# Performance work log

Hardware: AMD Instinct MI355X
Metric: run time of the kernel (lower is better)

Reference implementation:

```python
import jax, jax.numpy as jnp
import numpy as np

N = 262144   # occupied sparse voxels
C = 64       # channels
K3 = 27      # 3^3 kernel offsets (rulebook width)


def spconv(feats, W, nbr):
    """Submanifold sparse conv: gather -> matmul -> accumulate per kernel offset.
    feats: [N, Cin], W: [K3, Cin, Cout], nbr: [N, K3] int32 neighbor indices.
    """
    def step(acc, wi):
        w, idx = wi          # w: [Cin, Cout], idx: [N]
        return acc + feats[idx] @ w, None
    acc = jnp.zeros((feats.shape[0], W.shape[-1]), dtype=feats.dtype)
    out, _ = jax.lax.scan(step, acc, (W, nbr.T))
    return out


def inr(feats, nbr, w00, w01, w10, w11, w12):
    # branch 0: conv0_1(relu(conv0_0(x)))  (both k=3)
    out0 = spconv(jax.nn.relu(spconv(feats, w00, nbr)), w01, nbr)
    # branch 1: conv1_2(relu(conv1_1(relu(conv1_0(x)))))  (1x1, k=3, 1x1)
    out1 = jax.nn.relu(spconv(jax.nn.relu(feats @ w10), w11, nbr)) @ w12
    # concat halves back to C, residual add
    return jnp.concatenate([out0, out1], axis=1) + feats


def setup_inputs() -> dict:
    key = jax.random.key(0)
    ks = jax.random.split(key, 16)
    Ch = C // 2
    s3 = 1.0 / np.sqrt(K3 * C)
    s3h = 1.0 / np.sqrt(K3 * Ch)
    s1 = 1.0 / np.sqrt(C)
    s1h = 1.0 / np.sqrt(Ch)
    feats = jax.random.normal(ks[0], (N, C), dtype=jnp.float32)
    nbr = jax.random.randint(ks[1], (N, K3), 0, N, dtype=jnp.int32)
    w1 = jax.random.normal(ks[2], (K3, C, C), dtype=jnp.float32) * s3
    w2 = jax.random.normal(ks[3], (K3, C, C), dtype=jnp.float32) * s3
    # 3 stacked INR blocks
    b00 = jax.random.normal(ks[4], (3, K3, C, Ch), dtype=jnp.float32) * s3
    b01 = jax.random.normal(ks[5], (3, K3, Ch, Ch), dtype=jnp.float32) * s3h
    b10 = jax.random.normal(ks[6], (3, C, Ch), dtype=jnp.float32) * s1
    b11 = jax.random.normal(ks[7], (3, K3, Ch, Ch), dtype=jnp.float32) * s3h
    b12 = jax.random.normal(ks[8], (3, Ch, Ch), dtype=jnp.float32) * s1h
    return {"feats": feats, "nbr": nbr, "w1": w1, "w2": w2,
            "b00": b00, "b01": b01, "b10": b10, "b11": b11, "b12": b12}


def reference(feats, nbr, w1, w2, b00, b01, b10, b11, b12):
    x = jax.nn.relu(spconv(feats, w1, nbr))   # x = relu(conv1(x))
    h = x
    for i in range(3):
        h = inr(h, nbr, b00[i], b01[i], b10[i], b11[i], b12[i])
    out = h + x                                # block(x) + x
    return spconv(out, w2, nbr)                # conv2(out)
```

## Files before the change

### kernel.cpp

```cpp
#include <hip/hip_runtime.h>
#include <hip/hip_bf16.h>

typedef __attribute__((ext_vector_type(8))) __bf16 bf16x8;
typedef __attribute__((ext_vector_type(4))) float f32x4;

#define DEVI __device__ __forceinline__

static constexpr int NVOX = 262144;

DEVI unsigned short f2b_rne(float f) {
    unsigned int u = __float_as_uint(f);
    u = (u + 0x7fffu + ((u >> 16) & 1u)) >> 16;
    return (unsigned short)u;
}
DEVI float b2f(unsigned short h) {
    return __uint_as_float(((unsigned int)h) << 16);
}
DEVI bf16x8 ld8(const unsigned short* p) { return *reinterpret_cast<const bf16x8*>(p); }
DEVI f32x4 mfma16(bf16x8 a, bf16x8 b, f32x4 c) {
    return __builtin_amdgcn_mfma_f32_16x16x32_bf16(a, b, c, 0, 0, 0);
}

DEVI void stage16(const unsigned short* __restrict__ src, unsigned short* dst,
                  int n16, int tid, int nthr) {
    const float4* s = reinterpret_cast<const float4*>(src);
    float4* d = reinterpret_cast<float4*>(dst);
    for (int c = tid; c < n16; c += nthr) d[c] = s[c];
}


__global__ void f2b_kernel(const float* __restrict__ src, unsigned short* __restrict__ dst) {
    const size_t i = (size_t)(blockIdx.x * 256 + threadIdx.x) * 8;
    const float4 a = *reinterpret_cast<const float4*>(src + i);
    const float4 b = *reinterpret_cast<const float4*>(src + i + 4);
    union { unsigned short h[8]; uint4 v; } o;
    o.h[0] = f2b_rne(a.x); o.h[1] = f2b_rne(a.y); o.h[2] = f2b_rne(a.z); o.h[3] = f2b_rne(a.w);
    o.h[4] = f2b_rne(b.x); o.h[5] = f2b_rne(b.y); o.h[6] = f2b_rne(b.z); o.h[7] = f2b_rne(b.w);
    *reinterpret_cast<uint4*>(dst + i) = o.v;
}

__global__ void wconv_kernel(const float* __restrict__ src, unsigned short* __restrict__ dst,
                             int K, int Cin, int Cout) {
    const int KC = Cin >> 5, NT = Cout >> 4;
    const int total = K * KC * NT * 512;
    src += (size_t)blockIdx.y * K * Cin * Cout;
    dst += (size_t)blockIdx.y * total;
    for (int e = blockIdx.x * 256 + threadIdx.x; e < total; e += gridDim.x * 256) {
        const int j = e & 7;
        const int ln = (e >> 3) & 63;
        const int blob = e >> 9;
        const int nt = blob % NT;
        const int t = blob / NT;
        const int kc = t % KC;
        const int k = t / KC;
        const int cin = kc * 32 + (ln >> 4) * 8 + j;
        const int cout = nt * 16 + (ln & 15);
        dst[e] = f2b_rne(src[((size_t)k * Cin + cin) * Cout + cout]);
    }
}


template<bool RELU, bool OUTF32>
__global__ __launch_bounds__(1024)
void conv_full_kernel(const unsigned short* __restrict__ in,
                      const int* __restrict__ nbr,
                      const unsigned short* __restrict__ wf,
                      void* __restrict__ outv)
{
    __shared__ unsigned short wlds[7 * 8 * 512];
    const int tid = threadIdx.x;
    const int lane = tid & 63, wave = tid >> 6;
    const int lrow = lane & 15, lkg = lane >> 4;
    const int vb = blockIdx.x * 512 + wave * 32;

    constexpr int ID = 6;
    constexpr int GS = 3;

    const int* nrow0 = nbr + (size_t)(vb + lrow) * 27;
    const int* nrow1 = nbr + (size_t)(vb + 16 + lrow) * 27;

    int i0[ID], i1[ID];
    bf16x8 ga[GS][2][2];

#pragma unroll
    for (int t = 0; t < ID; ++t) { i0[t] = nrow0[t]; i1[t] = nrow1[t]; }
#pragma unroll
    for (int t = 0; t < 2; ++t) {
        const unsigned short* a0 = in + (size_t)i0[t] * 64 + lkg * 8;
        const unsigned short* a1 = in + (size_t)i1[t] * 64 + lkg * 8;
        ga[t][0][0] = ld8(a0); ga[t][0][1] = ld8(a0 + 32);
        ga[t][1][0] = ld8(a1); ga[t][1][1] = ld8(a1 + 32);
    }

    const f32x4 FZ = {0.f, 0.f, 0.f, 0.f};
    f32x4 acc[2][4];
#pragma unroll
    for (int m = 0; m < 2; ++m)
#pragma unroll
        for (int nt = 0; nt < 4; ++nt) acc[m][nt] = FZ;

#pragma unroll
    for (int t = 0; t < 27; ++t) {
        if (t % 7 == 0) {
            const int nk = (27 - t) < 7 ? (27 - t) : 7;
            __syncthreads();
            stage16(wf + (size_t)t * 8 * 512, wlds, nk * 8 * 64, tid, 1024);
            __syncthreads();
        }
        if (t + ID < 27) {
            i0[t % ID] = nrow0[t + ID];
            i1[t % ID] = nrow1[t + ID];
        }
        if (t + 2 < 27) {
            const int u = t + 2, s = u % GS;
            const unsigned short* a0 = in + (size_t)i0[u % ID] * 64 + lkg * 8;
            const unsigned short* a1 = in + (size_t)i1[u % ID] * 64 + lkg * 8;
            ga[s][0][0] = ld8(a0); ga[s][0][1] = ld8(a0 + 32);
            ga[s][1][0] = ld8(a1); ga[s][1][1] = ld8(a1 + 32);
        }
        const int kk = t % 7;
        const unsigned short* bl = wlds + kk * 8 * 512 + lane * 8;
        const int s = t % GS;
#pragma unroll
        for (int kc = 0; kc < 2; ++kc)
#pragma unroll
            for (int nt = 0; nt < 4; ++nt) {
                const bf16x8 bf = ld8(bl + (kc * 4 + nt) * 512);
                acc[0][nt] = mfma16(ga[s][0][kc], bf, acc[0][nt]);
                acc[1][nt] = mfma16(ga[s][1][kc], bf, acc[1][nt]);
            }
    }

#pragma unroll
    for (int m = 0; m < 2; ++m)
#pragma unroll
        for (int nt = 0; nt < 4; ++nt)
#pragma unroll
            for (int r = 0; r < 4; ++r) {
                const int v = vb + m * 16 + lkg * 4 + r;
                float val = acc[m][nt][r];
                if (RELU) val = fmaxf(val, 0.f);
                if (OUTF32)
                    reinterpret_cast<float*>(outv)[(size_t)v * 64 + nt * 16 + lrow] = val;
                else
                    reinterpret_cast<unsigned short*>(outv)[(size_t)v * 64 + nt * 16 + lrow] = f2b_rne(val);
            }
}

__global__ __launch_bounds__(1024)
void kernel_A(const unsigned short* __restrict__ h,
              const int* __restrict__ nbr,
              const unsigned short* __restrict__ b00f,
              const unsigned short* __restrict__ b10f,
              unsigned short* __restrict__ u)
{
    __shared__ unsigned short wlds[60 * 512];
    const int tid = threadIdx.x;
    const int lane = tid & 63, wave = tid >> 6;
    const int lrow = lane & 15, lkg = lane >> 4;
    const int vb = blockIdx.x * 512 + wave * 32;

    constexpr int ID = 6;
    constexpr int GS = 3;

    const int* nrow0 = nbr + (size_t)(vb + lrow) * 27;
    const int* nrow1 = nbr + (size_t)(vb + 16 + lrow) * 27;

    int i0[ID], i1[ID];
    bf16x8 ga[GS][2][2];

#pragma unroll
    for (int t = 0; t < ID; ++t) { i0[t] = nrow0[t]; i1[t] = nrow1[t]; }
#pragma unroll
    for (int t = 0; t < 2; ++t) {
        const unsigned short* a0 = h + (size_t)i0[t] * 64 + lkg * 8;
        const unsigned short* a1 = h + (size_t)i1[t] * 64 + lkg * 8;
        ga[t][0][0] = ld8(a0); ga[t][0][1] = ld8(a0 + 32);
        ga[t][1][0] = ld8(a1); ga[t][1][1] = ld8(a1 + 32);
    }

    const f32x4 FZ = {0.f, 0.f, 0.f, 0.f};
    f32x4 acc0[2][2], acc1[2][2];
#pragma unroll
    for (int m = 0; m < 2; ++m)
#pragma unroll
        for (int nt = 0; nt < 2; ++nt) { acc0[m][nt] = FZ; acc1[m][nt] = FZ; }

#pragma unroll
    for (int t = 0; t < 27; ++t) {
        if (t == 0) {
            __syncthreads();
            stage16(b00f, wlds, 14 * 4 * 64, tid, 1024);
            stage16(b10f, wlds + 56 * 512, 4 * 64, tid, 1024);
            __syncthreads();
        } else if (t == 14) {
            __syncthreads();
            stage16(b00f + (size_t)14 * 4 * 512, wlds, 13 * 4 * 64, tid, 1024);
            __syncthreads();
        }
        if (t + ID < 27) {
            i0[t % ID] = nrow0[t + ID];
            i1[t % ID] = nrow1[t + ID];
        }
        if (t + 2 < 27) {
            const int u2 = t + 2, s = u2 % GS;
            const unsigned short* a0 = h + (size_t)i0[u2 % ID] * 64 + lkg * 8;
            const unsigned short* a1 = h + (size_t)i1[u2 % ID] * 64 + lkg * 8;
            ga[s][0][0] = ld8(a0); ga[s][0][1] = ld8(a0 + 32);
            ga[s][1][0] = ld8(a1); ga[s][1][1] = ld8(a1 + 32);
        }
        const int kk = (t < 14) ? t : t - 14;
        const unsigned short* bl = wlds + kk * 4 * 512 + lane * 8;
        const int s = t % GS;
#pragma unroll
        for (int kc = 0; kc < 2; ++kc)
#pragma unroll
            for (int nt = 0; nt < 2; ++nt) {
                const bf16x8 bf = ld8(bl + (kc * 2 + nt) * 512);
                acc0[0][nt] = mfma16(ga[s][0][kc], bf, acc0[0][nt]);
                acc0[1][nt] = mfma16(ga[s][1][kc], bf, acc0[1][nt]);
            }
    }
    {
        const unsigned short* bl = wlds + 56 * 512 + lane * 8;
#pragma unroll
        for (int m = 0; m < 2; ++m) {
            const unsigned short* ar = h + (size_t)(vb + m * 16 + lrow) * 64;
#pragma unroll
            for (int kc = 0; kc < 2; ++kc) {
                const bf16x8 af = ld8(ar + kc * 32 + lkg * 8);
#pragma unroll
                for (int nt = 0; nt < 2; ++nt) {
                    const bf16x8 bf = ld8(bl + (kc * 2 + nt) * 512);
                    acc1[m][nt] = mfma16(af, bf, acc1[m][nt]);
                }
            }
        }
    }
#pragma unroll
    for (int m = 0; m < 2; ++m)
#pragma unroll
        for (int nt = 0; nt < 2; ++nt)
#pragma unroll
            for (int r = 0; r < 4; ++r) {
                const int v = vb + m * 16 + lkg * 4 + r;
                u[(size_t)v * 64 + nt * 16 + lrow] = f2b_rne(fmaxf(acc0[m][nt][r], 0.f));
                u[(size_t)v * 64 + 32 + nt * 16 + lrow] = f2b_rne(fmaxf(acc1[m][nt][r], 0.f));
            }
}

__global__ __launch_bounds__(1024)
void kernel_B(const unsigned short* __restrict__ u,
              const int* __restrict__ nbr,
              const unsigned short* __restrict__ b01f,
              const unsigned short* __restrict__ b11f,
              const unsigned short* __restrict__ b12f,
              const unsigned short* __restrict__ hres,
              const unsigned short* __restrict__ xres,
              unsigned short* __restrict__ hout)
{
    __shared__ unsigned short wlds[56 * 512];
    const int tid = threadIdx.x;
    const int lane = tid & 63, wave = tid >> 6;
    const int lrow = lane & 15, lkg = lane >> 4;
    const int vb = blockIdx.x * 512 + wave * 32;

    constexpr int ID = 6;
    constexpr int GS = 3;

    const int* nrow0 = nbr + (size_t)(vb + lrow) * 27;
    const int* nrow1 = nbr + (size_t)(vb + 16 + lrow) * 27;

    int i0[ID], i1[ID];
    bf16x8 ga[GS][2][2];

#pragma unroll
    for (int t = 0; t < ID; ++t) { i0[t] = nrow0[t]; i1[t] = nrow1[t]; }
#pragma unroll
    for (int t = 0; t < 2; ++t) {
        const unsigned short* a0 = u + (size_t)i0[t] * 64 + lkg * 8;
        const unsigned short* a1 = u + (size_t)i1[t] * 64 + lkg * 8;
        ga[t][0][0] = ld8(a0); ga[t][0][1] = ld8(a0 + 32);
        ga[t][1][0] = ld8(a1); ga[t][1][1] = ld8(a1 + 32);
    }

    const f32x4 FZ = {0.f, 0.f, 0.f, 0.f};
    f32x4 acc0[2][2], acc1[2][2];
#pragma unroll
    for (int m = 0; m < 2; ++m)
#pragma unroll
        for (int nt = 0; nt < 2; ++nt) { acc0[m][nt] = FZ; acc1[m][nt] = FZ; }

#pragma unroll
    for (int t = 0; t < 27; ++t) {
        if (t == 0) {
            __syncthreads();
            stage16(b01f, wlds, 14 * 2 * 64, tid, 1024);
            stage16(b11f, wlds + 28 * 512, 14 * 2 * 64, tid, 1024);
            __syncthreads();
        } else if (t == 14) {
            __syncthreads();
            stage16(b01f + (size_t)28 * 512, wlds, 13 * 2 * 64, tid, 1024);
            stage16(b11f + (size_t)28 * 512, wlds + 28 * 512, 13 * 2 * 64, tid, 1024);
            __syncthreads();
        }
        if (t + ID < 27) {
            i0[t % ID] = nrow0[t + ID];
            i1[t % ID] = nrow1[t + ID];
        }
        if (t + 2 < 27) {
            const int u2 = t + 2, s = u2 % GS;
            const unsigned short* a0 = u + (size_t)i0[u2 % ID] * 64 + lkg * 8;
            const unsigned short* a1 = u + (size_t)i1[u2 % ID] * 64 + lkg * 8;
            ga[s][0][0] = ld8(a0); ga[s][0][1] = ld8(a0 + 32);
            ga[s][1][0] = ld8(a1); ga[s][1][1] = ld8(a1 + 32);
        }
        const int kk = (t < 14) ? t : t - 14;
        const unsigned short* bl = wlds + lane * 8;
        const int s = t % GS;
#pragma unroll
        for (int nt = 0; nt < 2; ++nt) {
            const bf16x8 w01 = ld8(bl + (kk * 2 + nt) * 512);
            const bf16x8 w11 = ld8(bl + (28 + kk * 2 + nt) * 512);
            acc0[0][nt] = mfma16(ga[s][0][0], w01, acc0[0][nt]);
            acc0[1][nt] = mfma16(ga[s][1][0], w01, acc0[1][nt]);
            acc1[0][nt] = mfma16(ga[s][0][1], w11, acc1[0][nt]);
            acc1[1][nt] = mfma16(ga[s][1][1], w11, acc1[1][nt]);
        }
    }

    bf16x8 w12r[2];
#pragma unroll
    for (int nt = 0; nt < 2; ++nt) w12r[nt] = ld8(b12f + nt * 512 + lane * 8);

    __syncthreads();

    f32x4 out1[2][2];
    char* tb = reinterpret_cast<char*>(wlds) + wave * 1024;
#pragma unroll
    for (int m = 0; m < 2; ++m) {
#pragma unroll
        for (int nt = 0; nt < 2; ++nt)
#pragma unroll
            for (int r = 0; r < 4; ++r) {
                const int row = lkg * 4 + r;
                const int byte = (nt * 16 + lrow) * 2;
                const int off = row * 64 + (((byte >> 4) ^ (row & 3)) << 4) + (byte & 15);
                *reinterpret_cast<unsigned short*>(tb + off) = f2b_rne(fmaxf(acc1[m][nt][r], 0.f));
            }
        __syncthreads();
        const int roff = lrow * 64 + ((lkg ^ (lrow & 3)) << 4);
        const bf16x8 af2 = *reinterpret_cast<const bf16x8*>(tb + roff);
#pragma unroll
        for (int nt = 0; nt < 2; ++nt)
            out1[m][nt] = mfma16(af2, w12r[nt], FZ);
        __syncthreads();
    }

#pragma unroll
    for (int m = 0; m < 2; ++m)
#pragma unroll
        for (int nt = 0; nt < 2; ++nt)
#pragma unroll
            for (int r = 0; r < 4; ++r) {
                const int v = vb + m * 16 + lkg * 4 + r;
                const int c0 = nt * 16 + lrow;
                const int c1 = 32 + c0;
                float r0 = acc0[m][nt][r] + b2f(hres[(size_t)v * 64 + c0]);
                float r1 = out1[m][nt][r] + b2f(hres[(size_t)v * 64 + c1]);
                if (xres) {
                    r0 += b2f(xres[(size_t)v * 64 + c0]);
                    r1 += b2f(xres[(size_t)v * 64 + c1]);
                }
                hout[(size_t)v * 64 + c0] = f2b_rne(r0);
                hout[(size_t)v * 64 + c1] = f2b_rne(r1);
            }
}


extern "C" void kernel_launch(void* const* d_in, const int* in_sizes, int n_in,
                              void* d_out, int out_size, void* d_ws, size_t ws_size,
                              hipStream_t stream)
{
    const float* feats = (const float*)d_in[0];
    const int*   nbr   = (const int*)d_in[1];
    const float* w1    = (const float*)d_in[2];
    const float* w2    = (const float*)d_in[3];
    const float* b00   = (const float*)d_in[4];
    const float* b01   = (const float*)d_in[5];
    const float* b10   = (const float*)d_in[6];
    const float* b11   = (const float*)d_in[7];
    const float* b12   = (const float*)d_in[8];

    const size_t NC = (size_t)NVOX * 64;
    unsigned short* xbuf = (unsigned short*)d_ws;
    unsigned short* hbuf = xbuf + NC;
    unsigned short* wbuf = hbuf + NC;
    if (ws_size < (2 * NC + 562176) * sizeof(unsigned short)) return;

    unsigned short* fbuf = (unsigned short*)d_out;
    unsigned short* ubuf = fbuf + NC;

    const size_t OFF_W1 = 0, OFF_W2 = 110592, OFF_B00 = 221184, OFF_B01 = 387072,
                 OFF_B10 = 470016, OFF_B11 = 476160, OFF_B12 = 559104;

    f2b_kernel<<<8192, 256, 0, stream>>>(feats, fbuf);
    wconv_kernel<<<dim3(432, 1), 256, 0, stream>>>(w1, wbuf + OFF_W1, 27, 64, 64);
    wconv_kernel<<<dim3(432, 1), 256, 0, stream>>>(w2, wbuf + OFF_W2, 27, 64, 64);
    wconv_kernel<<<dim3(216, 3), 256, 0, stream>>>(b00, wbuf + OFF_B00, 27, 64, 32);
    wconv_kernel<<<dim3(108, 3), 256, 0, stream>>>(b01, wbuf + OFF_B01, 27, 32, 32);
    wconv_kernel<<<dim3(8, 3),   256, 0, stream>>>(b10, wbuf + OFF_B10, 1, 64, 32);
    wconv_kernel<<<dim3(108, 3), 256, 0, stream>>>(b11, wbuf + OFF_B11, 27, 32, 32);
    wconv_kernel<<<dim3(4, 3),   256, 0, stream>>>(b12, wbuf + OFF_B12, 1, 32, 32);

    conv_full_kernel<true, false><<<512, 1024, 0, stream>>>(fbuf, nbr, wbuf + OFF_W1, xbuf);

    for (int i = 0; i < 3; ++i) {
        kernel_A<<<512, 1024, 0, stream>>>(i ? hbuf : xbuf, nbr,
                                           wbuf + OFF_B00 + (size_t)i * 55296,
                                           wbuf + OFF_B10 + (size_t)i * 2048, ubuf);
        kernel_B<<<512, 1024, 0, stream>>>(ubuf, nbr,
                                           wbuf + OFF_B01 + (size_t)i * 27648,
                                           wbuf + OFF_B11 + (size_t)i * 27648,
                                           wbuf + OFF_B12 + (size_t)i * 1024,
                                           i ? hbuf : xbuf,
                                           (i == 2) ? xbuf : (const unsigned short*)nullptr,
                                           hbuf);
    }

    conv_full_kernel<false, true><<<512, 1024, 0, stream>>>(hbuf, nbr, wbuf + OFF_W2, d_out);
}
```

Measured before the change: 1.186 ms.

## Shrink per-wave voxel tile and blocks to raise occupancy in conv kernels

Each wave now handles 16 voxels instead of 32, and each block uses 512 threads covering 128 voxels, launched across 2048 blocks. The smaller LDS weight stages (5, 7 or 9 offsets) and fewer registers per thread are meant to allow several blocks per CU, so more waves can hide the latency of the random gather. In exchange, each block restages weights from global memory more often relative to the voxels it computes, and the B-fragment LDS reads are reused across only one M tile instead of two.

```diff
diff --git a/kernel.cpp b/kernel.cpp
--- a/kernel.cpp
+++ b/kernel.cpp
@@ -61,64 +61,54 @@
 
 
 template<bool RELU, bool OUTF32>
-__global__ __launch_bounds__(1024)
+__global__ __launch_bounds__(512, 7)
 void conv_full_kernel(const unsigned short* __restrict__ in,
                       const int* __restrict__ nbr,
                       const unsigned short* __restrict__ wf,
                       void* __restrict__ outv)
 {
-    __shared__ unsigned short wlds[7 * 8 * 512];
+    __shared__ unsigned short wlds[5 * 8 * 512];
     const int tid = threadIdx.x;
     const int lane = tid & 63, wave = tid >> 6;
     const int lrow = lane & 15, lkg = lane >> 4;
-    const int vb = blockIdx.x * 512 + wave * 32;
-
-    constexpr int ID = 6;
+    const int vb = blockIdx.x * 128 + wave * 16;
+
+    constexpr int ID = 4;
     constexpr int GS = 3;
 
-    const int* nrow0 = nbr + (size_t)(vb + lrow) * 27;
-    const int* nrow1 = nbr + (size_t)(vb + 16 + lrow) * 27;
-
-    int i0[ID], i1[ID];
-    bf16x8 ga[GS][2][2];
-
-#pragma unroll
-    for (int t = 0; t < ID; ++t) { i0[t] = nrow0[t]; i1[t] = nrow1[t]; }
+    const int* nrow = nbr + (size_t)(vb + lrow) * 27;
+
+    int i0[ID];
+    bf16x8 ga[GS][2];
+
+#pragma unroll
+    for (int t = 0; t < ID; ++t) i0[t] = nrow[t];
 #pragma unroll
     for (int t = 0; t < 2; ++t) {
         const unsigned short* a0 = in + (size_t)i0[t] * 64 + lkg * 8;
-        const unsigned short* a1 = in + (size_t)i1[t] * 64 + lkg * 8;
-        ga[t][0][0] = ld8(a0); ga[t][0][1] = ld8(a0 + 32);
-        ga[t][1][0] = ld8(a1); ga[t][1][1] = ld8(a1 + 32);
+        ga[t][0] = ld8(a0); ga[t][1] = ld8(a0 + 32);
     }
 
     const f32x4 FZ = {0.f, 0.f, 0.f, 0.f};
-    f32x4 acc[2][4];
-#pragma unroll
-    for (int m = 0; m < 2; ++m)
-#pragma unroll
-        for (int nt = 0; nt < 4; ++nt) acc[m][nt] = FZ;
+    f32x4 acc[4];
+#pragma unroll
+    for (int nt = 0; nt < 4; ++nt) acc[nt] = FZ;
 
 #pragma unroll
     for (int t = 0; t < 27; ++t) {
-        if (t % 7 == 0) {
-            const int nk = (27 - t) < 7 ? (27 - t) : 7;
-            __syncthreads();
-            stage16(wf + (size_t)t * 8 * 512, wlds, nk * 8 * 64, tid, 1024);
-            __syncthreads();
-        }
-        if (t + ID < 27) {
-            i0[t % ID] = nrow0[t + ID];
-            i1[t % ID] = nrow1[t + ID];
-        }
+        if (t % 5 == 0) {
+            const int nk = (27 - t) < 5 ? (27 - t) : 5;
+            __syncthreads();
+            stage16(wf + (size_t)t * 8 * 512, wlds, nk * 8 * 64, tid, 512);
+            __syncthreads();
+        }
+        if (t + ID < 27) i0[t % ID] = nrow[t + ID];
         if (t + 2 < 27) {
             const int u = t + 2, s = u % GS;
             const unsigned short* a0 = in + (size_t)i0[u % ID] * 64 + lkg * 8;
-            const unsigned short* a1 = in + (size_t)i1[u % ID] * 64 + lkg * 8;
-            ga[s][0][0] = ld8(a0); ga[s][0][1] = ld8(a0 + 32);
-            ga[s][1][0] = ld8(a1); ga[s][1][1] = ld8(a1 + 32);
-        }
-        const int kk = t % 7;
+            ga[s][0] = ld8(a0); ga[s][1] = ld8(a0 + 32);
+        }
+        const int kk = t % 5;
         const unsigned short* bl = wlds + kk * 8 * 512 + lane * 8;
         const int s = t % GS;
 #pragma unroll
@@ -126,90 +116,74 @@
 #pragma unroll
             for (int nt = 0; nt < 4; ++nt) {
                 const bf16x8 bf = ld8(bl + (kc * 4 + nt) * 512);
-                acc[0][nt] = mfma16(ga[s][0][kc], bf, acc[0][nt]);
-                acc[1][nt] = mfma16(ga[s][1][kc], bf, acc[1][nt]);
+                acc[nt] = mfma16(ga[s][kc], bf, acc[nt]);
             }
     }
 
 #pragma unroll
-    for (int m = 0; m < 2; ++m)
-#pragma unroll
-        for (int nt = 0; nt < 4; ++nt)
-#pragma unroll
-            for (int r = 0; r < 4; ++r) {
-                const int v = vb + m * 16 + lkg * 4 + r;
-                float val = acc[m][nt][r];
-                if (RELU) val = fmaxf(val, 0.f);
-                if (OUTF32)
-                    reinterpret_cast<float*>(outv)[(size_t)v * 64 + nt * 16 + lrow] = val;
-                else
-                    reinterpret_cast<unsigned short*>(outv)[(size_t)v * 64 + nt * 16 + lrow] = f2b_rne(val);
-            }
-}
-
-__global__ __launch_bounds__(1024)
+    for (int nt = 0; nt < 4; ++nt)
+#pragma unroll
+        for (int r = 0; r < 4; ++r) {
+            const int v = vb + lkg * 4 + r;
+            float val = acc[nt][r];
+            if (RELU) val = fmaxf(val, 0.f);
+            if (OUTF32)
+                reinterpret_cast<float*>(outv)[(size_t)v * 64 + nt * 16 + lrow] = val;
+            else
+                reinterpret_cast<unsigned short*>(outv)[(size_t)v * 64 + nt * 16 + lrow] = f2b_rne(val);
+        }
+}
+
+__global__ __launch_bounds__(512, 7)
 void kernel_A(const unsigned short* __restrict__ h,
               const int* __restrict__ nbr,
               const unsigned short* __restrict__ b00f,
               const unsigned short* __restrict__ b10f,
               unsigned short* __restrict__ u)
 {
-    __shared__ unsigned short wlds[60 * 512];
+    __shared__ unsigned short wlds[32 * 512];
     const int tid = threadIdx.x;
     const int lane = tid & 63, wave = tid >> 6;
     const int lrow = lane & 15, lkg = lane >> 4;
-    const int vb = blockIdx.x * 512 + wave * 32;
-
-    constexpr int ID = 6;
+    const int vb = blockIdx.x * 128 + wave * 16;
+
+    constexpr int ID = 4;
     constexpr int GS = 3;
 
-    const int* nrow0 = nbr + (size_t)(vb + lrow) * 27;
-    const int* nrow1 = nbr + (size_t)(vb + 16 + lrow) * 27;
-
-    int i0[ID], i1[ID];
-    bf16x8 ga[GS][2][2];
-
-#pragma unroll
-    for (int t = 0; t < ID; ++t) { i0[t] = nrow0[t]; i1[t] = nrow1[t]; }
+    const int* nrow = nbr + (size_t)(vb + lrow) * 27;
+
+    int i0[ID];
+    bf16x8 ga[GS][2];
+
+#pragma unroll
+    for (int t = 0; t < ID; ++t) i0[t] = nrow[t];
 #pragma unroll
     for (int t = 0; t < 2; ++t) {
         const unsigned short* a0 = h + (size_t)i0[t] * 64 + lkg * 8;
-        const unsigned short* a1 = h + (size_t)i1[t] * 64 + lkg * 8;
-        ga[t][0][0] = ld8(a0); ga[t][0][1] = ld8(a0 + 32);
-        ga[t][1][0] = ld8(a1); ga[t][1][1] = ld8(a1 + 32);
+        ga[t][0] = ld8(a0); ga[t][1] = ld8(a0 + 32);
     }
 
     const f32x4 FZ = {0.f, 0.f, 0.f, 0.f};
-    f32x4 acc0[2][2], acc1[2][2];
-#pragma unroll
-    for (int m = 0; m < 2; ++m)
-#pragma unroll
-        for (int nt = 0; nt < 2; ++nt) { acc0[m][nt] = FZ; acc1[m][nt] = FZ; }
+    f32x4 acc0[2];
+#pragma unroll
+    for (int nt = 0; nt < 2; ++nt) acc0[nt] = FZ;
 
 #pragma unroll
     for (int t = 0; t < 27; ++t) {
-        if (t == 0) {
-            __syncthreads();
-            stage16(b00f, wlds, 14 * 4 * 64, tid, 1024);
-            stage16(b10f, wlds + 56 * 512, 4 * 64, tid, 1024);
-            __syncthreads();
-        } else if (t == 14) {
-            __syncthreads();
-            stage16(b00f + (size_t)14 * 4 * 512, wlds, 13 * 4 * 64, tid, 1024);
-            __syncthreads();
-        }
-        if (t + ID < 27) {
-            i0[t % ID] = nrow0[t + ID];
-            i1[t % ID] = nrow1[t + ID];
-        }
+        if (t % 7 == 0) {
+            const int nk = (27 - t) < 7 ? (27 - t) : 7;
+            __syncthreads();
+            stage16(b00f + (size_t)t * 4 * 512, wlds, nk * 4 * 64, tid, 512);
+            if (t == 0) stage16(b10f, wlds + 28 * 512, 4 * 64, tid, 512);
+            __syncthreads();
+        }
+        if (t + ID < 27) i0[t % ID] = nrow[t + ID];
         if (t + 2 < 27) {
             const int u2 = t + 2, s = u2 % GS;
             const unsigned short* a0 = h + (size_t)i0[u2 % ID] * 64 + lkg * 8;
-            const unsigned short* a1 = h + (size_t)i1[u2 % ID] * 64 + lkg * 8;
-            ga[s][0][0] = ld8(a0); ga[s][0][1] = ld8(a0 + 32);
-            ga[s][1][0] = ld8(a1); ga[s][1][1] = ld8(a1 + 32);
-        }
-        const int kk = (t < 14) ? t : t - 14;
+            ga[s][0] = ld8(a0); ga[s][1] = ld8(a0 + 32);
+        }
+        const int kk = t % 7;
         const unsigned short* bl = wlds + kk * 4 * 512 + lane * 8;
         const int s = t % GS;
 #pragma unroll
@@ -217,39 +191,36 @@
 #pragma unroll
             for (int nt = 0; nt < 2; ++nt) {
                 const bf16x8 bf = ld8(bl + (kc * 2 + nt) * 512);
-                acc0[0][nt] = mfma16(ga[s][0][kc], bf, acc0[0][nt]);
-                acc0[1][nt] = mfma16(ga[s][1][kc], bf, acc0[1][nt]);
+                acc0[nt] = mfma16(ga[s][kc], bf, acc0[nt]);
             }
     }
+    f32x4 acc1[2];
+#pragma unroll
+    for (int nt = 0; nt < 2; ++nt) acc1[nt] = FZ;
     {
-        const unsigned short* bl = wlds + 56 * 512 + lane * 8;
-#pragma unroll
-        for (int m = 0; m < 2; ++m) {
-            const unsigned short* ar = h + (size_t)(vb + m * 16 + lrow) * 64;
-#pragma unroll
-            for (int kc = 0; kc < 2; ++kc) {
-                const bf16x8 af = ld8(ar + kc * 32 + lkg * 8);
-#pragma unroll
-                for (int nt = 0; nt < 2; ++nt) {
-                    const bf16x8 bf = ld8(bl + (kc * 2 + nt) * 512);
-                    acc1[m][nt] = mfma16(af, bf, acc1[m][nt]);
-                }
+        const unsigned short* bl = wlds + 28 * 512 + lane * 8;
+        const unsigned short* ar = h + (size_t)(vb + lrow) * 64;
+#pragma unroll
+        for (int kc = 0; kc < 2; ++kc) {
+            const bf16x8 af = ld8(ar + kc * 32 + lkg * 8);
+#pragma unroll
+            for (int nt = 0; nt < 2; ++nt) {
+                const bf16x8 bf = ld8(bl + (kc * 2 + nt) * 512);
+                acc1[nt] = mfma16(af, bf, acc1[nt]);
             }
         }
     }
 #pragma unroll
-    for (int m = 0; m < 2; ++m)
-#pragma unroll
-        for (int nt = 0; nt < 2; ++nt)
-#pragma unroll
-            for (int r = 0; r < 4; ++r) {
-                const int v = vb + m * 16 + lkg * 4 + r;
-                u[(size_t)v * 64 + nt * 16 + lrow] = f2b_rne(fmaxf(acc0[m][nt][r], 0.f));
-                u[(size_t)v * 64 + 32 + nt * 16 + lrow] = f2b_rne(fmaxf(acc1[m][nt][r], 0.f));
-            }
-}
-
-__global__ __launch_bounds__(1024)
+    for (int nt = 0; nt < 2; ++nt)
+#pragma unroll
+        for (int r = 0; r < 4; ++r) {
+            const int v = vb + lkg * 4 + r;
+            u[(size_t)v * 64 + nt * 16 + lrow] = f2b_rne(fmaxf(acc0[nt][r], 0.f));
+            u[(size_t)v * 64 + 32 + nt * 16 + lrow] = f2b_rne(fmaxf(acc1[nt][r], 0.f));
+        }
+}
+
+__global__ __launch_bounds__(512, 7)
 void kernel_B(const unsigned short* __restrict__ u,
               const int* __restrict__ nbr,
               const unsigned short* __restrict__ b01f,
@@ -259,73 +230,56 @@
               const unsigned short* __restrict__ xres,
               unsigned short* __restrict__ hout)
 {
-    __shared__ unsigned short wlds[56 * 512];
+    __shared__ unsigned short wlds[36 * 512];
     const int tid = threadIdx.x;
     const int lane = tid & 63, wave = tid >> 6;
     const int lrow = lane & 15, lkg = lane >> 4;
-    const int vb = blockIdx.x * 512 + wave * 32;
-
-    constexpr int ID = 6;
+    const int vb = blockIdx.x * 128 + wave * 16;
+
+    constexpr int ID = 4;
     constexpr int GS = 3;
 
-    const int* nrow0 = nbr + (size_t)(vb + lrow) * 27;
-    const int* nrow1 = nbr + (size_t)(vb + 16 + lrow) * 27;
-
-    int i0[ID], i1[ID];
-    bf16x8 ga[GS][2][2];
-
-#pragma unroll
-    for (int t = 0; t < ID; ++t) { i0[t] = nrow0[t]; i1[t] = nrow1[t]; }
+    const int* nrow = nbr + (size_t)(vb + lrow) * 27;
+
+    int i0[ID];
+    bf16x8 ga[GS][2];
+
+#pragma unroll
+    for (int t = 0; t < ID; ++t) i0[t] = nrow[t];
 #pragma unroll
     for (int t = 0; t < 2; ++t) {
         const unsigned short* a0 = u + (size_t)i0[t] * 64 + lkg * 8;
-        const unsigned short* a1 = u + (size_t)i1[t] * 64 + lkg * 8;
-        ga[t][0][0] = ld8(a0); ga[t][0][1] = ld8(a0 + 32);
-        ga[t][1][0] = ld8(a1); ga[t][1][1] = ld8(a1 + 32);
+        ga[t][0] = ld8(a0); ga[t][1] = ld8(a0 + 32);
     }
 
     const f32x4 FZ = {0.f, 0.f, 0.f, 0.f};
-    f32x4 acc0[2][2], acc1[2][2];
-#pragma unroll
-    for (int m = 0; m < 2; ++m)
-#pragma unroll
-        for (int nt = 0; nt < 2; ++nt) { acc0[m][nt] = FZ; acc1[m][nt] = FZ; }
+    f32x4 acc0[2], acc1[2];
+#pragma unroll
+    for (int nt = 0; nt < 2; ++nt) { acc0[nt] = FZ; acc1[nt] = FZ; }
 
 #pragma unroll
     for (int t = 0; t < 27; ++t) {
-        if (t == 0) {
-            __syncthreads();
-            stage16(b01f, wlds, 14 * 2 * 64, tid, 1024);
-            stage16(b11f, wlds + 28 * 512, 14 * 2 * 64, tid, 1024);
-            __syncthreads();
-        } else if (t == 14) {
-            __syncthreads();
-            stage16(b01f + (size_t)28 * 512, wlds, 13 * 2 * 64, tid, 1024);
-            stage16(b11f + (size_t)28 * 512, wlds + 28 * 512, 13 * 2 * 64, tid, 1024);
-            __syncthreads();
-        }
-        if (t + ID < 27) {
-            i0[t % ID] = nrow0[t + ID];
-            i1[t % ID] = nrow1[t + ID];
-        }
+        if (t % 9 == 0) {
+            __syncthreads();
+            stage16(b01f + (size_t)t * 2 * 512, wlds, 9 * 2 * 64, tid, 512);
+            stage16(b11f + (size_t)t * 2 * 512, wlds + 18 * 512, 9 * 2 * 64, tid, 512);
+            __syncthreads();
+        }
+        if (t + ID < 27) i0[t % ID] = nrow[t + ID];
         if (t + 2 < 27) {
             const int u2 = t + 2, s = u2 % GS;
             const unsigned short* a0 = u + (size_t)i0[u2 % ID] * 64 + lkg * 8;
-            const unsigned short* a1 = u + (size_t)i1[u2 % ID] * 64 + lkg * 8;
-            ga[s][0][0] = ld8(a0); ga[s][0][1] = ld8(a0 + 32);
-            ga[s][1][0] = ld8(a1); ga[s][1][1] = ld8(a1 + 32);
-        }
-        const int kk = (t < 14) ? t : t - 14;
+            ga[s][0] = ld8(a0); ga[s][1] = ld8(a0 + 32);
+        }
+        const int kk = t % 9;
         const unsigned short* bl = wlds + lane * 8;
         const int s = t % GS;
 #pragma unroll
         for (int nt = 0; nt < 2; ++nt) {
             const bf16x8 w01 = ld8(bl + (kk * 2 + nt) * 512);
-            const bf16x8 w11 = ld8(bl + (28 + kk * 2 + nt) * 512);
-            acc0[0][nt] = mfma16(ga[s][0][0], w01, acc0[0][nt]);
-            acc0[1][nt] = mfma16(ga[s][1][0], w01, acc0[1][nt]);
-            acc1[0][nt] = mfma16(ga[s][0][1], w11, acc1[0][nt]);
-            acc1[1][nt] = mfma16(ga[s][1][1], w11, acc1[1][nt]);
+            const bf16x8 w11 = ld8(bl + (18 * 512) + (kk * 2 + nt) * 512);
+            acc0[nt] = mfma16(ga[s][0], w01, acc0[nt]);
+            acc1[nt] = mfma16(ga[s][1], w11, acc1[nt]);
         }
     }
 
@@ -335,46 +289,42 @@
 
     __syncthreads();
 
-    f32x4 out1[2][2];
+    f32x4 out1[2];
     char* tb = reinterpret_cast<char*>(wlds) + wave * 1024;
 #pragma unroll
-    for (int m = 0; m < 2; ++m) {
-#pragma unroll
-        for (int nt = 0; nt < 2; ++nt)
-#pragma unroll
-            for (int r = 0; r < 4; ++r) {
-                const int row = lkg * 4 + r;
-                const int byte = (nt * 16 + lrow) * 2;
-                const int off = row * 64 + (((byte >> 4) ^ (row & 3)) << 4) + (byte & 15);
-                *reinterpret_cast<unsigned short*>(tb + off) = f2b_rne(fmaxf(acc1[m][nt][r], 0.f));
-            }
-        __syncthreads();
+    for (int nt = 0; nt < 2; ++nt)
+#pragma unroll
+        for (int r = 0; r < 4; ++r) {
+            const int row = lkg * 4 + r;
+            const int byte = (nt * 16 + lrow) * 2;
+            const int off = row * 64 + (((byte >> 4) ^ (row & 3)) << 4) + (byte & 15);
+            *reinterpret_cast<unsigned short*>(tb + off) = f2b_rne(fmaxf(acc1[nt][r], 0.f));
+        }
+    __syncthreads();
+    {
         const int roff = lrow * 64 + ((lkg ^ (lrow & 3)) << 4);
         const bf16x8 af2 = *reinterpret_cast<const bf16x8*>(tb + roff);
 #pragma unroll
         for (int nt = 0; nt < 2; ++nt)
-            out1[m][nt] = mfma16(af2, w12r[nt], FZ);
-        __syncthreads();
-    }
-
-#pragma unroll
-    for (int m = 0; m < 2; ++m)
-#pragma unroll
-        for (int nt = 0; nt < 2; ++nt)
-#pragma unroll
-            for (int r = 0; r < 4; ++r) {
-                const int v = vb + m * 16 + lkg * 4 + r;
-                const int c0 = nt * 16 + lrow;
-                const int c1 = 32 + c0;
-                float r0 = acc0[m][nt][r] + b2f(hres[(size_t)v * 64 + c0]);
-                float r1 = out1[m][nt][r] + b2f(hres[(size_t)v * 64 + c1]);
-                if (xres) {
-                    r0 += b2f(xres[(size_t)v * 64 + c0]);
-                    r1 += b2f(xres[(size_t)v * 64 + c1]);
-                }
-                hout[(size_t)v * 64 + c0] = f2b_rne(r0);
-                hout[(size_t)v * 64 + c1] = f2b_rne(r1);
+            out1[nt] = mfma16(af2, w12r[nt], FZ);
+    }
+
+#pragma unroll
+    for (int nt = 0; nt < 2; ++nt)
+#pragma unroll
+        for (int r = 0; r < 4; ++r) {
+            const int v = vb + lkg * 4 + r;
+            const int c0 = nt * 16 + lrow;
+            const int c1 = 32 + c0;
+            float r0 = acc0[nt][r] + b2f(hres[(size_t)v * 64 + c0]);
+            float r1 = out1[nt][r] + b2f(hres[(size_t)v * 64 + c1]);
+            if (xres) {
+                r0 += b2f(xres[(size_t)v * 64 + c0]);
+                r1 += b2f(xres[(size_t)v * 64 + c1]);
             }
+            hout[(size_t)v * 64 + c0] = f2b_rne(r0);
+            hout[(size_t)v * 64 + c1] = f2b_rne(r1);
+        }
 }
 
 
@@ -413,13 +363,13 @@
     wconv_kernel<<<dim3(108, 3), 256, 0, stream>>>(b11, wbuf + OFF_B11, 27, 32, 32);
     wconv_kernel<<<dim3(4, 3),   256, 0, stream>>>(b12, wbuf + OFF_B12, 1, 32, 32);
 
-    conv_full_kernel<true, false><<<512, 1024, 0, stream>>>(fbuf, nbr, wbuf + OFF_W1, xbuf);
+    conv_full_kernel<true, false><<<2048, 512, 0, stream>>>(fbuf, nbr, wbuf + OFF_W1, xbuf);
 
     for (int i = 0; i < 3; ++i) {
-        kernel_A<<<512, 1024, 0, stream>>>(i ? hbuf : xbuf, nbr,
+        kernel_A<<<2048, 512, 0, stream>>>(i ? hbuf : xbuf, nbr,
                                            wbuf + OFF_B00 + (size_t)i * 55296,
                                            wbuf + OFF_B10 + (size_t)i * 2048, ubuf);
-        kernel_B<<<512, 1024, 0, stream>>>(ubuf, nbr,
+        kernel_B<<<2048, 512, 0, stream>>>(ubuf, nbr,
                                            wbuf + OFF_B01 + (size_t)i * 27648,
                                            wbuf + OFF_B11 + (size_t)i * 27648,
                                            wbuf + OFF_B12 + (size_t)i * 1024,
@@ -428,5 +378,5 @@
                                            hbuf);
     }
 
-    conv_full_kernel<false, true><<<512, 1024, 0, stream>>>(hbuf, nbr, wbuf + OFF_W2, d_out);
-}
+    conv_full_kernel<false, true><<<2048, 512, 0, stream>>>(hbuf, nbr, wbuf + OFF_W2, d_out);
+}
```

Measured after the change: 1.209 ms. About the same (+1.9%).
